# Performance work log

Hardware: AMD Instinct MI355X
Metric: run time of the kernel (lower is better)

Reference implementation:

```python
import jax, jax.numpy as jnp
import numpy as np

B, S, H, F, E, K = 2, 2048, 1024, 4096, 8, 2


def setup_inputs() -> dict:
    key = jax.random.key(0)
    ks = jax.random.split(key, 6)
    x = jax.random.normal(ks[0], (B, S, H), dtype=jnp.float32)
    probs = jax.random.uniform(ks[1], (K, B, S, 1), dtype=jnp.float32)
    experts = jax.random.randint(ks[2], (K, B, S, 1), 0, E, dtype=jnp.int32)
    # per-expert FFN params; 0.02 scale mimics typical transformer init
    w1 = jax.random.normal(ks[3], (E, H, F), dtype=jnp.float32) * 0.02
    b1 = jnp.zeros((E, F), dtype=jnp.float32)
    w2 = jax.random.normal(ks[4], (E, F, H), dtype=jnp.float32) * 0.02
    b2 = jnp.zeros((E, H), dtype=jnp.float32)
    return {"x": x, "probs": probs, "experts": experts,
            "w1": w1, "b1": b1, "w2": w2, "b2": b2}


def reference(x, probs, experts, w1, b1, w2, b2):
    # Dense compute-all-experts FFN: every expert processes every token.
    h = jnp.einsum('bsh,ehf->ebsf', x, w1) + b1[:, None, None, :]  # [E,B,S,F]
    h = jax.nn.gelu(h)
    y = jnp.einsum('ebsf,efh->ebsh', h, w2) + b2[:, None, None, :]  # [E,B,S,H]
    # Masked combine: sum_e sum_j probs_j * y_e * (experts_j == e)
    onehot = jax.nn.one_hot(experts[..., 0], w1.shape[0], dtype=x.dtype)  # [K,B,S,E]
    weights = jnp.einsum('kbsl,kbse->bse', probs, onehot)  # [B,S,E]
    out = jnp.einsum('bse,ebsh->bsh', weights, y)
    return out
```

## Files before the change

kernel.cpp:

```cpp
#include <hip/hip_runtime.h>
#include <stdint.h>

#define H_DIM 1024
#define F_DIM 4096
#define E_NUM 8
#define T_NUM 4096
#define NE    8192
#define BM    256
#define BN    128
#define BK    64
#define MAXT  39
#define PADM  (MAXT*BM)
#define TBY   49152
#define LDSSZ (3*TBY)

#define M_NT  0
#define M_PB  1
#define M_CNT 16
#define M_CUR 24
#define M_TE  32
#define M_TR  72
#define M_INTS 112

typedef float  f32x4  __attribute__((ext_vector_type(4)));
typedef short  bf16x8 __attribute__((ext_vector_type(8)));
typedef __bf16 b16v8  __attribute__((ext_vector_type(8)));
typedef unsigned short u16;
typedef u16    u16x8  __attribute__((ext_vector_type(8)));

#define BAR() __builtin_amdgcn_s_barrier()

__device__ __forceinline__ float gelu_tanh(float v) {
  float u = 0.7978845608028654f * (v + 0.044715f * v * v * v);
  return v / (1.0f + __expf(-2.0f * u));
}

__device__ __forceinline__ float b2f(u16 v) {
  union { float f; unsigned u; } x; x.u = ((unsigned)v) << 16; return x.f;
}

__device__ __forceinline__ void gl16(const void* g, void* l) {
  __builtin_amdgcn_global_load_lds(
      (const __attribute__((address_space(1))) unsigned int*)g,
      (__attribute__((address_space(3))) unsigned int*)l, 16, 0, 0);
}


__global__ void k_init(int* tok, float* wgt, int* meta) {
  int i = blockIdx.x * 256 + threadIdx.x;
  if (i < PADM) { tok[i] = 0; wgt[i] = 0.f; }
  if (i < E_NUM) { meta[M_CNT + i] = 0; meta[M_CUR + i] = 0; }
}

__global__ void k_count(const int* __restrict__ experts, int* meta) {
  int i = blockIdx.x * 256 + threadIdx.x;
  int e = experts[i];
  int lane = threadIdx.x & 63;
#pragma unroll
  for (int ee = 0; ee < E_NUM; ++ee) {
    unsigned long long bm = __ballot(e == ee);
    if (e == ee && lane == __builtin_ctzll(bm))
      atomicAdd(&meta[M_CNT + ee], __popcll(bm));
  }
}

__global__ void k_plan(int* meta) {
  if (threadIdx.x != 0 || blockIdx.x != 0) return;
  int pb = 0, idx = 0;
  for (int e = 0; e < E_NUM; ++e) {
    int c = meta[M_CNT + e];
    int nt = (c + BM - 1) / BM;
    meta[M_PB + e] = pb;
    for (int t = 0; t < nt && idx < MAXT; ++t) {
      meta[M_TE + idx] = e; meta[M_TR + idx] = pb + t * BM; ++idx;
    }
    pb += nt * BM;
  }
  meta[M_NT] = idx;
}

__global__ void k_scatter(const int* __restrict__ experts, const float* __restrict__ probs,
                          int* tok, float* wgt, int* entpos, int* meta) {
  int i = blockIdx.x * 256 + threadIdx.x;
  int e = experts[i];
  int t = i & (T_NUM - 1);
  float p = probs[i];
  int lane = threadIdx.x & 63;
#pragma unroll
  for (int ee = 0; ee < E_NUM; ++ee) {
    unsigned long long bm = __ballot(e == ee);
    if (e == ee) {
      int leader = __builtin_ctzll(bm);
      int cnt = __popcll(bm);
      int base = 0;
      if (lane == leader) base = atomicAdd(&meta[M_CUR + ee], cnt);
      base = __shfl(base, leader);
      int rank = __popcll(bm & ((1ull << lane) - 1ull));
      int pos = meta[M_PB + ee] + base + rank;
      tok[pos] = t;
      wgt[pos] = p;
      entpos[i] = pos;
    }
  }
}

__global__ void k_cvt_x(const float* __restrict__ x, u16* __restrict__ xbf) {
  int i = blockIdx.x * 256 + threadIdx.x;
  const f32x4* xp = (const f32x4*)x;
  f32x4 a = xp[i * 2], b = xp[i * 2 + 1];
  b16v8 o;
  o[0] = (__bf16)a[0]; o[1] = (__bf16)a[1]; o[2] = (__bf16)a[2]; o[3] = (__bf16)a[3];
  o[4] = (__bf16)b[0]; o[5] = (__bf16)b[1]; o[6] = (__bf16)b[2]; o[7] = (__bf16)b[3];
  ((b16v8*)xbf)[i] = o;
}

__global__ __launch_bounds__(256) void k_trans(const float* __restrict__ W, u16* __restrict__ Wt,
                                               int R, int C) {
  alignas(16) __shared__ char L[16384];
  int e = blockIdx.z;
  int r0 = blockIdx.y * 64, c0 = blockIdx.x * 64;
  const float* We = W + (size_t)e * R * C;
  u16* Wte = Wt + (size_t)e * R * C;
  int tid = threadIdx.x;
#pragma unroll
  for (int it = 0; it < 4; ++it) {
    int gi = it * 256 + tid;
    int row = gi >> 4, c4 = gi & 15;
    f32x4 v = *(const f32x4*)(We + (size_t)(r0 + row) * C + c0 + c4 * 4);
    *(f32x4*)(L + row * 256 + ((c4 ^ (row & 15)) * 16)) = v;
  }
  __syncthreads();
#pragma unroll
  for (int s = 0; s < 2; ++s) {
    int chunk = s * 256 + tid;
    int c = chunk >> 3, rb = chunk & 7;
    b16v8 o;
#pragma unroll
    for (int j = 0; j < 8; ++j) {
      int r = rb * 8 + j;
      float f = *(const float*)(L + r * 256 + (((c >> 2) ^ (r & 15)) * 16) + (c & 3) * 4);
      o[j] = (__bf16)f;
    }
    *(b16v8*)(void*)(Wte + (size_t)(c0 + c) * R + r0 + rb * 8) = o;
  }
}


#define STG_A(kt, sbase, j) gl16(asrc[j] + (size_t)(kt) * BK, LDS + (sbase) + (j) * 8192 + wid * 1024)
#define STG_B(kt, sbase, j) gl16(bsrc[j] + (size_t)(kt) * BK, LDS + (sbase) + 32768 + (j) * 8192 + wid * 1024)

#define STAGEALL(kt, sbase)                                                   \
  { _Pragma("unroll") for (int j = 0; j < 4; ++j) STG_A(kt, sbase, j);        \
    _Pragma("unroll") for (int j = 0; j < 2; ++j) STG_B(kt, sbase, j); }

#define PHASE(sbase, kk, STAGES)                                              \
  { asm volatile("" ::: "memory");                                           \
    const char* Ab_ = LDS + (sbase);                                         \
    const char* Bb_ = LDS + (sbase) + 32768;                                 \
    int kbyte = (kk) * 64 + ((lane >> 4) << 4);                              \
    bf16x8 af[4], bfr[4];                                                    \
    _Pragma("unroll") for (int m = 0; m < 4; ++m) {                          \
      int r = wr * 64 + m * 16 + (lane & 15);                                \
      af[m] = *(const bf16x8*)(Ab_ + r * 128 + (kbyte ^ ((r & 7) << 4)));    \
    }                                                                        \
    _Pragma("unroll") for (int n = 0; n < 4; ++n) {                          \
      int c = wc * 64 + n * 16 + (lane & 15);                                \
      bfr[n] = *(const bf16x8*)(Bb_ + c * 128 + (kbyte ^ ((c & 7) << 4)));   \
    }                                                                        \
    STAGES;                                                                  \
    asm volatile("" ::: "memory");                                           \
    BAR();                                                                   \
    __builtin_amdgcn_s_setprio(1);                                           \
    _Pragma("unroll") for (int m = 0; m < 4; ++m)                            \
      _Pragma("unroll") for (int n = 0; n < 4; ++n)                          \
        acc[m][n] = __builtin_amdgcn_mfma_f32_16x16x32_bf16(af[m], bfr[n], acc[m][n], 0, 0, 0); \
    __builtin_amdgcn_s_setprio(0);                                           \
  }

#define GEMM_KLOOP(NT)                                                        \
  STAGEALL(0, 0)                                                              \
  STAGEALL(1, TBY)                                                            \
  { int sb = 0, s2 = 2 * TBY;                                                 \
    for (int t = 0; t < (NT); ++t) {                                          \
      if (t == (NT) - 1) { asm volatile("s_waitcnt vmcnt(0)" ::: "memory"); } \
      else               { asm volatile("s_waitcnt vmcnt(6)" ::: "memory"); } \
      BAR();                                                                  \
      bool st_ = (t + 2 < (NT));                                              \
      PHASE(sb, 0, if (st_) { STG_A(t + 2, s2, 0); STG_A(t + 2, s2, 1); STG_A(t + 2, s2, 2); }) \
      PHASE(sb, 1, if (st_) { STG_A(t + 2, s2, 3); STG_B(t + 2, s2, 0); STG_B(t + 2, s2, 1); }) \
      sb = (sb == 2 * TBY) ? 0 : sb + TBY;                                    \
      s2 = (s2 == 2 * TBY) ? 0 : s2 + TBY;                                    \
    } }                                                                       \
  BAR();


__global__ __launch_bounds__(512, 1) void k_gemm1(
    const u16* __restrict__ xbf, const u16* __restrict__ wbuf, const float* __restrict__ b1,
    const int* __restrict__ tok, const int* __restrict__ meta, u16* __restrict__ hbuf)
{
  extern __shared__ char LDS[];
  int wg = blockIdx.x;
  int work = (wg & 7) * 156 + (wg >> 3);
  int slot = work % MAXT;
  int cbase = (work / MAXT) * BN;
  int nt = meta[M_NT];
  if (slot >= nt) return;
  int e     = meta[M_TE + slot];
  int rbase = meta[M_TR + slot];

  int tid = threadIdx.x;
  int lane = tid & 63;
  int wid = tid >> 6;
  int wr = wid >> 1, wc = wid & 1;
  int cc = tid & 7, rr = tid >> 3;

  const u16* asrc[4]; const u16* bsrc[2];
#pragma unroll
  for (int j = 0; j < 4; ++j) {
    int rj = j * 64 + rr;
    int t = tok[rbase + rj];
    asrc[j] = xbf + (size_t)t * H_DIM + ((cc ^ (rj & 7)) * 8);
  }
#pragma unroll
  for (int j = 0; j < 2; ++j) {
    int nj = j * 64 + rr;
    bsrc[j] = wbuf + ((size_t)e * F_DIM + cbase + nj) * H_DIM + ((cc ^ (nj & 7)) * 8);
  }

  f32x4 acc[4][4];
#pragma unroll
  for (int m = 0; m < 4; ++m)
#pragma unroll
    for (int n = 0; n < 4; ++n) acc[m][n] = (f32x4){0.f, 0.f, 0.f, 0.f};

  GEMM_KLOOP(H_DIM / BK)

  float bv[4];
#pragma unroll
  for (int n = 0; n < 4; ++n) bv[n] = b1[e * F_DIM + cbase + wc * 64 + n * 16 + (lane & 15)];
  char* reg = LDS + wid * 8192;
#pragma unroll
  for (int m = 0; m < 4; ++m)
#pragma unroll
    for (int n = 0; n < 4; ++n)
#pragma unroll
      for (int q = 0; q < 4; ++q) {
        float v = acc[m][n][q] + bv[n];
        v = gelu_tanh(v);
        int row4 = ((lane >> 4) << 2) + q;
        int col = n * 16 + (lane & 15);
        *(__bf16*)(reg + m * 2048 + row4 * 128 + col * 2) = (__bf16)v;
      }
#pragma unroll
  for (int q = 0; q < 8; ++q) {
    int m = q >> 1, p = q & 1;
    int byte = p * 1024 + lane * 16;
    u16x8 v = *(const u16x8*)(reg + m * 2048 + byte);
    int row  = p * 8 + (lane >> 3);
    int colb = (lane & 7) * 16;
    size_t grow = (size_t)(rbase + wr * 64 + m * 16 + row);
    size_t gcol = (size_t)(cbase + wc * 64 + (colb >> 1));
    *(u16x8*)(hbuf + grow * F_DIM + gcol) = v;
  }
}


__global__ __launch_bounds__(512, 1) void k_gemm2(
    const u16* __restrict__ hbuf, const u16* __restrict__ wbuf, const float* __restrict__ b2,
    const int* __restrict__ meta, u16* __restrict__ ybuf)
{
  extern __shared__ char LDS[];
  int wg = blockIdx.x;
  int work = (wg & 7) * 78 + (wg >> 3);
  int zi   = work / 312;
  int rem  = work % 312;
  int slot = rem % MAXT;
  int cbase = (rem / MAXT) * BN;
  int kzb   = zi * (F_DIM / 2);
  int nt = meta[M_NT];
  if (slot >= nt) return;
  int e     = meta[M_TE + slot];
  int rbase = meta[M_TR + slot];

  int tid = threadIdx.x;
  int lane = tid & 63;
  int wid = tid >> 6;
  int wr = wid >> 1, wc = wid & 1;
  int cc = tid & 7, rr = tid >> 3;

  const u16* asrc[4]; const u16* bsrc[2];
#pragma unroll
  for (int j = 0; j < 4; ++j) {
    int rj = j * 64 + rr;
    asrc[j] = hbuf + (size_t)(rbase + rj) * F_DIM + kzb + ((cc ^ (rj & 7)) * 8);
  }
#pragma unroll
  for (int j = 0; j < 2; ++j) {
    int nj = j * 64 + rr;
    bsrc[j] = wbuf + ((size_t)e * H_DIM + cbase + nj) * F_DIM + kzb + ((cc ^ (nj & 7)) * 8);
  }

  f32x4 acc[4][4];
#pragma unroll
  for (int m = 0; m < 4; ++m)
#pragma unroll
    for (int n = 0; n < 4; ++n) acc[m][n] = (f32x4){0.f, 0.f, 0.f, 0.f};

  GEMM_KLOOP((F_DIM / 2) / BK)

  bool z0 = (zi == 0);
  u16* yb = ybuf + (size_t)zi * PADM * H_DIM;
  float bv[4];
#pragma unroll
  for (int n = 0; n < 4; ++n)
    bv[n] = z0 ? b2[e * H_DIM + cbase + wc * 64 + n * 16 + (lane & 15)] : 0.f;
  char* reg = LDS + wid * 8192;
#pragma unroll
  for (int m = 0; m < 4; ++m)
#pragma unroll
    for (int n = 0; n < 4; ++n)
#pragma unroll
      for (int q = 0; q < 4; ++q) {
        float v = acc[m][n][q] + bv[n];
        int row4 = ((lane >> 4) << 2) + q;
        int col = n * 16 + (lane & 15);
        *(__bf16*)(reg + m * 2048 + row4 * 128 + col * 2) = (__bf16)v;
      }
#pragma unroll
  for (int q = 0; q < 8; ++q) {
    int m = q >> 1, p = q & 1;
    int byte = p * 1024 + lane * 16;
    u16x8 v = *(const u16x8*)(reg + m * 2048 + byte);
    int row  = p * 8 + (lane >> 3);
    int colb = (lane & 7) * 16;
    size_t grow = (size_t)(rbase + wr * 64 + m * 16 + row);
    size_t gcol = (size_t)(cbase + wc * 64 + (colb >> 1));
    *(u16x8*)(yb + grow * H_DIM + gcol) = v;
  }
}


__global__ __launch_bounds__(256) void k_combine(
    const u16* __restrict__ ybuf, const float* __restrict__ wgt,
    const int* __restrict__ entpos, float* __restrict__ out)
{
  int idx = blockIdx.x * 256 + threadIdx.x;
  int t = idx >> 7, hc = idx & 127;
  int p0 = entpos[t], p1 = entpos[T_NUM + t];
  float w0 = wgt[p0], w1 = wgt[p1];
  const u16x8* y0 = (const u16x8*)(ybuf);
  const u16x8* y1 = (const u16x8*)(ybuf + (size_t)PADM * H_DIM);
  u16x8 a = y0[(size_t)p0 * (H_DIM / 8) + hc];
  u16x8 b = y1[(size_t)p0 * (H_DIM / 8) + hc];
  u16x8 c = y0[(size_t)p1 * (H_DIM / 8) + hc];
  u16x8 d = y1[(size_t)p1 * (H_DIM / 8) + hc];
  f32x4 o0, o1;
#pragma unroll
  for (int j = 0; j < 4; ++j)
    o0[j] = w0 * (b2f(a[j]) + b2f(b[j])) + w1 * (b2f(c[j]) + b2f(d[j]));
#pragma unroll
  for (int j = 0; j < 4; ++j)
    o1[j] = w0 * (b2f(a[4 + j]) + b2f(b[4 + j])) + w1 * (b2f(c[4 + j]) + b2f(d[4 + j]));
  f32x4* op = (f32x4*)(out + (size_t)t * H_DIM + hc * 8);
  op[0] = o0;
  op[1] = o1;
}


extern "C" void kernel_launch(void* const* d_in, const int* in_sizes, int n_in,
                              void* d_out, int out_size, void* d_ws, size_t ws_size,
                              hipStream_t stream)
{
  const float* x       = (const float*)d_in[0];
  const float* probs   = (const float*)d_in[1];
  const int*   experts = (const int*)d_in[2];
  const float* w1      = (const float*)d_in[3];
  const float* b1      = (const float*)d_in[4];
  const float* w2      = (const float*)d_in[5];
  const float* b2      = (const float*)d_in[6];
  float* out = (float*)d_out;

  char* ws = (char*)d_ws;
  size_t off = 0;
  u16*   hbuf = (u16*)(ws + off);  off += (size_t)PADM * F_DIM * sizeof(u16);
  u16*   xbf  = (u16*)(ws + off);  off += (size_t)T_NUM * H_DIM * sizeof(u16);
  u16*   wbuf = (u16*)(ws + off);  off += (size_t)E_NUM * F_DIM * H_DIM * sizeof(u16);
  u16*   ybuf = (u16*)(ws + off);  off += (size_t)2 * PADM * H_DIM * sizeof(u16);
  int*   tok  = (int*)(ws + off);  off += (size_t)PADM * sizeof(int);
  float* wgt  = (float*)(ws + off); off += (size_t)PADM * sizeof(float);
  int*   entpos = (int*)(ws + off); off += (size_t)NE * sizeof(int);
  int*   meta = (int*)(ws + off);  off += M_INTS * sizeof(int);
  (void)ws_size; (void)in_sizes; (void)n_in;

  hipFuncSetAttribute(reinterpret_cast<const void*>(&k_gemm1),
                      hipFuncAttributeMaxDynamicSharedMemorySize, LDSSZ);
  hipFuncSetAttribute(reinterpret_cast<const void*>(&k_gemm2),
                      hipFuncAttributeMaxDynamicSharedMemorySize, LDSSZ);

  k_init   <<<dim3(PADM / 256), 256, 0, stream>>>(tok, wgt, meta);
  k_count  <<<dim3(NE / 256), 256, 0, stream>>>(experts, meta);
  k_plan   <<<1, 1, 0, stream>>>(meta);
  k_scatter<<<dim3(NE / 256), 256, 0, stream>>>(experts, probs, tok, wgt, entpos, meta);
  k_cvt_x  <<<dim3(T_NUM * H_DIM / 8 / 256), 256, 0, stream>>>(x, xbf);
  k_trans  <<<dim3(F_DIM / 64, H_DIM / 64, E_NUM), 256, 0, stream>>>(w1, wbuf, H_DIM, F_DIM);
  k_gemm1  <<<dim3(MAXT * (F_DIM / BN)), 512, LDSSZ, stream>>>(xbf, wbuf, b1, tok, meta, hbuf);
  k_trans  <<<dim3(H_DIM / 64, F_DIM / 64, E_NUM), 256, 0, stream>>>(w2, wbuf, F_DIM, H_DIM);
  k_gemm2  <<<dim3(MAXT * (H_DIM / BN) * 2), 512, LDSSZ, stream>>>(hbuf, wbuf, b2, meta, ybuf);
  k_combine<<<dim3(T_NUM * H_DIM / 8 / 256), 256, 0, stream>>>(ybuf, wgt, entpos, out);
}
```

Before: 356.6 us.

## Enlarge expert GEMM tiles to 256x256 with double-buffered LDS pipeline

Doubles the N tile of both expert GEMMs so each workgroup computes a 256x256 output block, with waves arranged 2x4 and each wave holding a 128x64 accumulator. The three-stage prefetch pipeline with split-phase staging is replaced by a simpler two-buffer scheme that waits for all loads and barriers every K step. Launch bounds now request two blocks per CU. The aim is more data reuse per loaded byte and fewer blocks. The risks are register pressure, since the accumulators alone take many registers under the tighter bound and may spill, plus less load/compute overlap, and 128KB of LDS per block may still allow only one block per CU. The init kernel is also renamed to take the experts input it does not use, with an extra barrier.

Result: no change. 356.4 us (-0.1%).

```diff
diff --git a/kernel.cpp b/kernel.cpp
--- a/kernel.cpp
+++ b/kernel.cpp
@@ -7,12 +7,12 @@
 #define T_NUM 4096
 #define NE    8192
 #define BM    256
-#define BN    128
+#define BN    256
 #define BK    64
 #define MAXT  39
 #define PADM  (MAXT*BM)
-#define TBY   49152
-#define LDSSZ (3*TBY)
+#define TBY   65536
+#define LDSSZ (2*TBY)
 
 #define M_NT  0
 #define M_PB  1
@@ -46,10 +46,11 @@
 }
 
 
-__global__ void k_init(int* tok, float* wgt, int* meta) {
+__global__ void k_init_count(const int* __restrict__ experts, int* tok, float* wgt, int* meta) {
   int i = blockIdx.x * 256 + threadIdx.x;
   if (i < PADM) { tok[i] = 0; wgt[i] = 0.f; }
   if (i < E_NUM) { meta[M_CNT + i] = 0; meta[M_CUR + i] = 0; }
+  __syncthreads();
 }
 
 __global__ void k_count(const int* __restrict__ experts, int* meta) {
@@ -146,61 +147,60 @@
 }
 
 
-#define STG_A(kt, sbase, j) gl16(asrc[j] + (size_t)(kt) * BK, LDS + (sbase) + (j) * 8192 + wid * 1024)
-#define STG_B(kt, sbase, j) gl16(bsrc[j] + (size_t)(kt) * BK, LDS + (sbase) + 32768 + (j) * 8192 + wid * 1024)
-
-#define STAGEALL(kt, sbase)                                                   \
-  { _Pragma("unroll") for (int j = 0; j < 4; ++j) STG_A(kt, sbase, j);        \
-    _Pragma("unroll") for (int j = 0; j < 2; ++j) STG_B(kt, sbase, j); }
-
-#define PHASE(sbase, kk, STAGES)                                              \
-  { asm volatile("" ::: "memory");                                           \
-    const char* Ab_ = LDS + (sbase);                                         \
-    const char* Bb_ = LDS + (sbase) + 32768;                                 \
-    int kbyte = (kk) * 64 + ((lane >> 4) << 4);                              \
-    bf16x8 af[4], bfr[4];                                                    \
-    _Pragma("unroll") for (int m = 0; m < 4; ++m) {                          \
-      int r = wr * 64 + m * 16 + (lane & 15);                                \
-      af[m] = *(const bf16x8*)(Ab_ + r * 128 + (kbyte ^ ((r & 7) << 4)));    \
-    }                                                                        \
-    _Pragma("unroll") for (int n = 0; n < 4; ++n) {                          \
-      int c = wc * 64 + n * 16 + (lane & 15);                                \
-      bfr[n] = *(const bf16x8*)(Bb_ + c * 128 + (kbyte ^ ((c & 7) << 4)));   \
-    }                                                                        \
-    STAGES;                                                                  \
-    asm volatile("" ::: "memory");                                           \
-    BAR();                                                                   \
-    __builtin_amdgcn_s_setprio(1);                                           \
-    _Pragma("unroll") for (int m = 0; m < 4; ++m)                            \
-      _Pragma("unroll") for (int n = 0; n < 4; ++n)                          \
-        acc[m][n] = __builtin_amdgcn_mfma_f32_16x16x32_bf16(af[m], bfr[n], acc[m][n], 0, 0, 0); \
-    __builtin_amdgcn_s_setprio(0);                                           \
-  }
+#define STAGEALL(kt, sb)                                                      \
+  { _Pragma("unroll")                                                         \
+    for (int j = 0; j < 4; ++j)                                               \
+      gl16(asrc[j] + (size_t)(kt) * BK, LDS + (sb) + j * 8192 + wid * 1024);  \
+    _Pragma("unroll")                                                         \
+    for (int j = 0; j < 4; ++j)                                               \
+      gl16(bsrc[j] + (size_t)(kt) * BK, LDS + (sb) + 32768 + j * 8192 + wid * 1024); }
+
+#define GEMM_COMPUTE(bb)                                                      \
+  { const char* Ab_ = LDS + (bb); const char* Bb_ = LDS + (bb) + 32768;       \
+    _Pragma("unroll")                                                         \
+    for (int kk = 0; kk < 2; ++kk) {                                          \
+      int kbyte = kk * 64 + ((lane >> 4) << 4);                               \
+      bf16x8 af[8], bfr[4];                                                   \
+      _Pragma("unroll")                                                       \
+      for (int m = 0; m < 8; ++m) {                                           \
+        int r = wr * 128 + m * 16 + (lane & 15);                              \
+        af[m] = *(const bf16x8*)(Ab_ + r * 128 + (kbyte ^ ((r & 7) << 4)));   \
+      }                                                                       \
+      _Pragma("unroll")                                                       \
+      for (int n = 0; n < 4; ++n) {                                           \
+        int c = wc * 64 + n * 16 + (lane & 15);                               \
+        bfr[n] = *(const bf16x8*)(Bb_ + c * 128 + (kbyte ^ ((c & 7) << 4)));  \
+      }                                                                       \
+      __builtin_amdgcn_s_setprio(1);                                          \
+      _Pragma("unroll")                                                       \
+      for (int m = 0; m < 8; ++m)                                             \
+        _Pragma("unroll")                                                     \
+        for (int n = 0; n < 4; ++n)                                           \
+          acc[m][n] = __builtin_amdgcn_mfma_f32_16x16x32_bf16(af[m], bfr[n], acc[m][n], 0, 0, 0); \
+      __builtin_amdgcn_s_setprio(0);                                          \
+    } }
 
 #define GEMM_KLOOP(NT)                                                        \
-  STAGEALL(0, 0)                                                              \
-  STAGEALL(1, TBY)                                                            \
-  { int sb = 0, s2 = 2 * TBY;                                                 \
-    for (int t = 0; t < (NT); ++t) {                                          \
-      if (t == (NT) - 1) { asm volatile("s_waitcnt vmcnt(0)" ::: "memory"); } \
-      else               { asm volatile("s_waitcnt vmcnt(6)" ::: "memory"); } \
+  STAGEALL(0, 0);                                                             \
+  asm volatile("s_waitcnt vmcnt(0)" ::: "memory");                            \
+  BAR();                                                                      \
+  { int cur = 0;                                                              \
+    for (int kt = 0; kt < (NT); ++kt) {                                       \
+      if (kt + 1 < (NT)) STAGEALL(kt + 1, (cur ^ 1) * TBY);                   \
+      GEMM_COMPUTE(cur * TBY);                                                \
+      asm volatile("s_waitcnt vmcnt(0)" ::: "memory");                        \
       BAR();                                                                  \
-      bool st_ = (t + 2 < (NT));                                              \
-      PHASE(sb, 0, if (st_) { STG_A(t + 2, s2, 0); STG_A(t + 2, s2, 1); STG_A(t + 2, s2, 2); }) \
-      PHASE(sb, 1, if (st_) { STG_A(t + 2, s2, 3); STG_B(t + 2, s2, 0); STG_B(t + 2, s2, 1); }) \
-      sb = (sb == 2 * TBY) ? 0 : sb + TBY;                                    \
-      s2 = (s2 == 2 * TBY) ? 0 : s2 + TBY;                                    \
-    } }                                                                       \
-  BAR();
-
-
-__global__ __launch_bounds__(512, 1) void k_gemm1(
+      cur ^= 1;                                                               \
+    } }
+
+
+__global__ __launch_bounds__(512, 2) void k_gemm1(
     const u16* __restrict__ xbf, const u16* __restrict__ wbuf, const float* __restrict__ b1,
     const int* __restrict__ tok, const int* __restrict__ meta, u16* __restrict__ hbuf)
 {
   extern __shared__ char LDS[];
   int wg = blockIdx.x;
-  int work = (wg & 7) * 156 + (wg >> 3);
+  int work = (wg & 7) * 78 + (wg >> 3);
   int slot = work % MAXT;
   int cbase = (work / MAXT) * BN;
   int nt = meta[M_NT];
@@ -211,25 +211,21 @@
   int tid = threadIdx.x;
   int lane = tid & 63;
   int wid = tid >> 6;
-  int wr = wid >> 1, wc = wid & 1;
+  int wr = wid >> 2, wc = wid & 3;
   int cc = tid & 7, rr = tid >> 3;
 
-  const u16* asrc[4]; const u16* bsrc[2];
+  const u16* asrc[4]; const u16* bsrc[4];
 #pragma unroll
   for (int j = 0; j < 4; ++j) {
     int rj = j * 64 + rr;
     int t = tok[rbase + rj];
     asrc[j] = xbf + (size_t)t * H_DIM + ((cc ^ (rj & 7)) * 8);
-  }
-#pragma unroll
-  for (int j = 0; j < 2; ++j) {
-    int nj = j * 64 + rr;
-    bsrc[j] = wbuf + ((size_t)e * F_DIM + cbase + nj) * H_DIM + ((cc ^ (nj & 7)) * 8);
-  }
-
-  f32x4 acc[4][4];
-#pragma unroll
-  for (int m = 0; m < 4; ++m)
+    bsrc[j] = wbuf + ((size_t)e * F_DIM + cbase + rj) * H_DIM + ((cc ^ (rj & 7)) * 8);
+  }
+
+  f32x4 acc[8][4];
+#pragma unroll
+  for (int m = 0; m < 8; ++m)
 #pragma unroll
     for (int n = 0; n < 4; ++n) acc[m][n] = (f32x4){0.f, 0.f, 0.f, 0.f};
 
@@ -238,9 +234,9 @@
   float bv[4];
 #pragma unroll
   for (int n = 0; n < 4; ++n) bv[n] = b1[e * F_DIM + cbase + wc * 64 + n * 16 + (lane & 15)];
-  char* reg = LDS + wid * 8192;
-#pragma unroll
-  for (int m = 0; m < 4; ++m)
+  char* reg = LDS + wid * 16384;
+#pragma unroll
+  for (int m = 0; m < 8; ++m)
 #pragma unroll
     for (int n = 0; n < 4; ++n)
 #pragma unroll
@@ -252,28 +248,28 @@
         *(__bf16*)(reg + m * 2048 + row4 * 128 + col * 2) = (__bf16)v;
       }
 #pragma unroll
-  for (int q = 0; q < 8; ++q) {
+  for (int q = 0; q < 16; ++q) {
     int m = q >> 1, p = q & 1;
     int byte = p * 1024 + lane * 16;
     u16x8 v = *(const u16x8*)(reg + m * 2048 + byte);
     int row  = p * 8 + (lane >> 3);
     int colb = (lane & 7) * 16;
-    size_t grow = (size_t)(rbase + wr * 64 + m * 16 + row);
+    size_t grow = (size_t)(rbase + wr * 128 + m * 16 + row);
     size_t gcol = (size_t)(cbase + wc * 64 + (colb >> 1));
     *(u16x8*)(hbuf + grow * F_DIM + gcol) = v;
   }
 }
 
 
-__global__ __launch_bounds__(512, 1) void k_gemm2(
+__global__ __launch_bounds__(512, 2) void k_gemm2(
     const u16* __restrict__ hbuf, const u16* __restrict__ wbuf, const float* __restrict__ b2,
     const int* __restrict__ meta, u16* __restrict__ ybuf)
 {
   extern __shared__ char LDS[];
   int wg = blockIdx.x;
-  int work = (wg & 7) * 78 + (wg >> 3);
-  int zi   = work / 312;
-  int rem  = work % 312;
+  int work = (wg & 7) * 39 + (wg >> 3);
+  int zi   = work / 156;
+  int rem  = work % 156;
   int slot = rem % MAXT;
   int cbase = (rem / MAXT) * BN;
   int kzb   = zi * (F_DIM / 2);
@@ -285,24 +281,20 @@
   int tid = threadIdx.x;
   int lane = tid & 63;
   int wid = tid >> 6;
-  int wr = wid >> 1, wc = wid & 1;
+  int wr = wid >> 2, wc = wid & 3;
   int cc = tid & 7, rr = tid >> 3;
 
-  const u16* asrc[4]; const u16* bsrc[2];
+  const u16* asrc[4]; const u16* bsrc[4];
 #pragma unroll
   for (int j = 0; j < 4; ++j) {
     int rj = j * 64 + rr;
     asrc[j] = hbuf + (size_t)(rbase + rj) * F_DIM + kzb + ((cc ^ (rj & 7)) * 8);
-  }
-#pragma unroll
-  for (int j = 0; j < 2; ++j) {
-    int nj = j * 64 + rr;
-    bsrc[j] = wbuf + ((size_t)e * H_DIM + cbase + nj) * F_DIM + kzb + ((cc ^ (nj & 7)) * 8);
-  }
-
-  f32x4 acc[4][4];
-#pragma unroll
-  for (int m = 0; m < 4; ++m)
+    bsrc[j] = wbuf + ((size_t)e * H_DIM + cbase + rj) * F_DIM + kzb + ((cc ^ (rj & 7)) * 8);
+  }
+
+  f32x4 acc[8][4];
+#pragma unroll
+  for (int m = 0; m < 8; ++m)
 #pragma unroll
     for (int n = 0; n < 4; ++n) acc[m][n] = (f32x4){0.f, 0.f, 0.f, 0.f};
 
@@ -314,9 +306,9 @@
 #pragma unroll
   for (int n = 0; n < 4; ++n)
     bv[n] = z0 ? b2[e * H_DIM + cbase + wc * 64 + n * 16 + (lane & 15)] : 0.f;
-  char* reg = LDS + wid * 8192;
-#pragma unroll
-  for (int m = 0; m < 4; ++m)
+  char* reg = LDS + wid * 16384;
+#pragma unroll
+  for (int m = 0; m < 8; ++m)
 #pragma unroll
     for (int n = 0; n < 4; ++n)
 #pragma unroll
@@ -327,13 +319,13 @@
         *(__bf16*)(reg + m * 2048 + row4 * 128 + col * 2) = (__bf16)v;
       }
 #pragma unroll
-  for (int q = 0; q < 8; ++q) {
+  for (int q = 0; q < 16; ++q) {
     int m = q >> 1, p = q & 1;
     int byte = p * 1024 + lane * 16;
     u16x8 v = *(const u16x8*)(reg + m * 2048 + byte);
     int row  = p * 8 + (lane >> 3);
     int colb = (lane & 7) * 16;
-    size_t grow = (size_t)(rbase + wr * 64 + m * 16 + row);
+    size_t grow = (size_t)(rbase + wr * 128 + m * 16 + row);
     size_t gcol = (size_t)(cbase + wc * 64 + (colb >> 1));
     *(u16x8*)(yb + grow * H_DIM + gcol) = v;
   }
@@ -397,7 +389,7 @@
   hipFuncSetAttribute(reinterpret_cast<const void*>(&k_gemm2),
                       hipFuncAttributeMaxDynamicSharedMemorySize, LDSSZ);
 
-  k_init   <<<dim3(PADM / 256), 256, 0, stream>>>(tok, wgt, meta);
+  k_init_count<<<dim3(PADM / 256), 256, 0, stream>>>(experts, tok, wgt, meta);
   k_count  <<<dim3(NE / 256), 256, 0, stream>>>(experts, meta);
   k_plan   <<<1, 1, 0, stream>>>(meta);
   k_scatter<<<dim3(NE / 256), 256, 0, stream>>>(experts, probs, tok, wgt, entpos, meta);
```
